# Kernel tuning notes

Hardware: AMD Instinct MI355X
Metric: run time of the kernel (lower is better)

The kernel has to match this reference:

```python
import jax, jax.numpy as jnp
import numpy as np

EPS = 1e-8


def corr1d(x, f, axis):
    """Centered 1-D correlation with filter f along `axis`, edge-padded."""
    k = f.shape[0]
    pad = k // 2
    padw = [(0, 0)] * x.ndim
    padw[axis] = (pad, pad)
    xp = jnp.pad(x, padw, mode='edge')
    n = x.shape[axis]
    out = jnp.zeros_like(x)
    for i in range(k):  # k is a small static filter size (3)
        sl = [slice(None)] * x.ndim
        sl[axis] = slice(i, i + n)
        out = out + f[i] * xp[tuple(sl)]
    return out


def conv2d_same(x, k2d):
    # x: [B,1,H,W], k2d: [kh,kw]
    return jax.lax.conv_general_dilated(x, k2d[None, None], (1, 1), 'SAME')


def setup_inputs() -> dict:
    key = jax.random.key(0)
    mosaick = jax.random.uniform(key, (16, 1, 1024, 1024), dtype=jnp.float32)
    # parameter inits exactly as in the torch module (sizes 3)
    gfilt = jnp.zeros((3,), jnp.float32).at[0].set(0.5).at[2].set(0.5)
    grad_filt = jnp.zeros((3,), jnp.float32).at[0].set(-1.0).at[2].set(1.0)
    return {"mosaick": mosaick, "gfilt": gfilt, "grad_filt": grad_filt}


def reference(mosaick, gfilt, grad_filt):
    m = mosaick  # [B,1,H,W], GRBG Bayer pattern
    B, _, H, W = m.shape
    yy, xx = jnp.meshgrid(jnp.arange(H), jnp.arange(W), indexing='ij')
    is_g = ((xx % 2) == (yy % 2)).astype(m.dtype)[None, None]          # green sites
    mask_r = (((yy % 2) == 0) & ((xx % 2) == 1)).astype(m.dtype)[None, None]
    mask_b = (((yy % 2) == 1) & ((xx % 2) == 0)).astype(m.dtype)[None, None]

    # learnable gradient measure (horizontal / vertical)
    dx = corr1d(m, grad_filt, axis=3)
    dy = corr1d(m, grad_filt, axis=2)
    # learnable green interpolation candidates
    gh = corr1d(m, gfilt, axis=3)
    gv = corr1d(m, gfilt, axis=2)

    adx, ady = jnp.abs(dx), jnp.abs(dy)
    w = ady / (adx + ady + EPS)          # big |dy| -> interpolate horizontally
    g_interp = w * gh + (1.0 - w) * gv
    green = is_g * m + (1.0 - is_g) * g_interp  # [B,1,H,W]

    # chroma reconstruction: bilinear interpolation of color differences
    K = jnp.array([[0.25, 0.5, 0.25],
                   [0.5, 1.0, 0.5],
                   [0.25, 0.5, 0.25]], m.dtype)

    def interp_chroma(mask):
        sparse = (m - green) * mask
        num = conv2d_same(sparse, K)
        den = conv2d_same(mask, K)  # mask is [1,1,H,W]; broadcasts in division
        return num / (den + EPS)

    red = green + interp_chroma(mask_r)
    blue = green + interp_chroma(mask_b)
    return jnp.concatenate([red, green, blue], axis=1)  # [B,3,H,W]
```

## Files before the change

kernel.cpp:

```cpp
#include <hip/hip_runtime.h>

#define HH 1024
#define WW 1024
#define TSX 128
#define TILE_H 64
#define ROWS_PW 16
#define SMW 134
#define SMH (TILE_H + 4)
#define EPSF 1e-8f

__device__ __forceinline__ float rcpf(float x) { return __builtin_amdgcn_rcpf(x); }

__global__ __launch_bounds__(256) void demosaick(
    const float* __restrict__ mos,
    const float* __restrict__ gfilt,
    const float* __restrict__ gradf,
    float* __restrict__ out)
{
    __shared__ __align__(16) float SM[SMH * SMW];
    const int tid  = threadIdx.x;
    const int lane = tid & 63;
    const int wv   = tid >> 6;
    const int bx = blockIdx.x, by = blockIdx.y, bz = blockIdx.z;
    const int gx0 = bx * TSX;
    const int gy0 = by * TILE_H;
    const size_t plane = (size_t)HH * WW;
    const float* __restrict__ src = mos + (size_t)bz * plane;

    const float gf0 = gfilt[0], gf1 = gfilt[1], gf2 = gfilt[2];
    const float df0 = gradf[0], df1 = gradf[1], df2 = gradf[2];

    for (int i = tid; i < SMH * (TSX + 4); i += 256) {
        int r = i / (TSX + 4);
        int c = i - r * (TSX + 4);
        int gy = min(max(gy0 - 2 + r, 0), HH - 1);
        int gx = min(max(gx0 - 2 + c, 0), WW - 1);
        SM[r * SMW + c] = src[(size_t)gy * WW + gx];
    }
    __syncthreads();

    const int ry0 = gy0 + wv * ROWS_PW;
    const int sr0 = wv * ROWS_PW;

    auto load_row = [&](int smr, float* d) {
        const float2* p = reinterpret_cast<const float2*>(&SM[smr * SMW + 2 * lane]);
        float2 a = p[0], b2 = p[1], c2 = p[2];
        d[0] = a.x; d[1] = a.y; d[2] = b2.x; d[3] = b2.y; d[4] = c2.x; d[5] = c2.y;
    };
    auto gi_at = [&](const float* up, const float* mid, const float* dn, int j) -> float {
        float xl = mid[j - 1], xc = mid[j], xr = mid[j + 1];
        float yu = up[j], yd = dn[j];
        float dx = df0 * xl + df1 * xc + df2 * xr;
        float dy = df0 * yu + df1 * xc + df2 * yd;
        float gh = gf0 * xl + gf1 * xc + gf2 * xr;
        float gv = gf0 * yu + gf1 * xc + gf2 * yd;
        float adx = fabsf(dx), ady = fabsf(dy);
        float w = ady * rcpf(adx + ady + EPSF);
        return w * gh + (1.0f - w) * gv;
    };
    auto green_row = [&](int gy, const float* up, const float* mid, const float* dn, float* G) {
        if (gy & 1) {
            G[0] = mid[1]; G[2] = mid[3];
            G[1] = gi_at(up, mid, dn, 2);
            G[3] = gi_at(up, mid, dn, 4);
        } else {
            G[1] = mid[2]; G[3] = mid[4];
            G[0] = gi_at(up, mid, dn, 1);
            G[2] = gi_at(up, mid, dn, 3);
        }
    };

    float A[6], Mm1[6], M0[6], Mp1[6], Mp2[6];
    float Gm1[4], G0[4], Gp1[4];
    load_row(sr0 + 0, A);
    load_row(sr0 + 1, Mm1);
    load_row(sr0 + 2, M0);
    load_row(sr0 + 3, Mp1);
    green_row(ry0 - 1, A, Mm1, M0, Gm1);
    green_row(ry0,     Mm1, M0, Mp1, G0);

    const int x0 = gx0 + 2 * lane;
    const float wL = (x0 - 1 >= 0) ? 1.0f : 0.0f;
    const float wR = (x0 + 2 < WW) ? 1.0f : 0.0f;
    float* __restrict__ obase = out + (size_t)bz * 3 * plane + (size_t)x0;

    #pragma unroll 4
    for (int r = 0; r < ROWS_PW; ++r) {
        const int y = ry0 + r;
        load_row(sr0 + r + 4, Mp2);
        green_row(y + 1, M0, Mp1, Mp2, Gp1);

        const float fU = (y > 0) ? 1.0f : 0.0f;
        const float fD = (y < HH - 1) ? 1.0f : 0.0f;
        const float g0 = G0[1], g1 = G0[2];
        const float m0 = M0[2], m1 = M0[3];
        float r0, b0, r1, b1;
        if ((y & 1) == 0) {
            {
                float dL = M0[1] - G0[0], dR = M0[3] - G0[2];
                r0 = g0 + (0.5f * (wL * dL + dR)) * rcpf(0.5f * (wL + 1.0f) + EPSF);
                float dU = Mm1[2] - Gm1[1], dD = Mp1[2] - Gp1[1];
                b0 = g0 + (0.5f * (fU * dU + fD * dD)) * rcpf(0.5f * (fU + fD) + EPSF);
            }
            {
                r1 = m1;
                float dUL = Mm1[2] - Gm1[1], dUR = Mm1[4] - Gm1[3];
                float dDL = Mp1[2] - Gp1[1], dDR = Mp1[4] - Gp1[3];
                float num = 0.25f * (fU * (dUL + wR * dUR) + fD * (dDL + wR * dDR));
                float den = 0.25f * ((fU + fD) * (1.0f + wR));
                b1 = g1 + num * rcpf(den + EPSF);
            }
        } else {
            {
                b0 = m0;
                float dUL = Mm1[1] - Gm1[0], dUR = Mm1[3] - Gm1[2];
                float dDL = Mp1[1] - Gp1[0], dDR = Mp1[3] - Gp1[2];
                float num = 0.25f * (fU * (wL * dUL + dUR) + fD * (wL * dDL + dDR));
                float den = 0.25f * ((fU + fD) * (wL + 1.0f));
                r0 = g0 + num * rcpf(den + EPSF);
            }
            {
                float dU = Mm1[3] - Gm1[2], dD = Mp1[3] - Gp1[2];
                r1 = g1 + (0.5f * (fU * dU + fD * dD)) * rcpf(0.5f * (fU + fD) + EPSF);
                float dL = M0[2] - G0[1], dR = M0[4] - G0[3];
                b1 = g1 + (0.5f * (dL + wR * dR)) * rcpf(0.5f * (1.0f + wR) + EPSF);
            }
        }

        float* prow = obase + (size_t)y * WW;
        *reinterpret_cast<float2*>(prow)             = make_float2(r0, r1);
        *reinterpret_cast<float2*>(prow + plane)     = make_float2(g0, g1);
        *reinterpret_cast<float2*>(prow + 2 * plane) = make_float2(b0, b1);

        #pragma unroll
        for (int j = 0; j < 6; ++j) { Mm1[j] = M0[j]; M0[j] = Mp1[j]; Mp1[j] = Mp2[j]; }
        #pragma unroll
        for (int j = 0; j < 4; ++j) { Gm1[j] = G0[j]; G0[j] = Gp1[j]; }
    }
}

extern "C" void kernel_launch(void* const* d_in, const int* in_sizes, int n_in,
                              void* d_out, int out_size, void* d_ws, size_t ws_size,
                              hipStream_t stream) {
    const float* mos = (const float*)d_in[0];
    const float* gf  = (const float*)d_in[1];
    const float* df  = (const float*)d_in[2];
    float* o = (float*)d_out;
    int B = in_sizes[0] / (HH * WW);
    dim3 grid(WW / TSX, HH / TILE_H, B);
    demosaick<<<grid, dim3(256, 1, 1), 0, stream>>>(mos, gf, df, o);
}
```

Before: 271.2 us.

## Drop shared-memory staging; read rows directly from global, 4 pixels per thread

Removes the LDS tile and its __syncthreads, so each thread loads its input rows straight from global memory as a float4 plus float2 halos, using a sliding register window over 16 rows. Each thread now produces 4 output pixels per row and writes them as float4 stores, and one block covers a full 1024-wide row strip. A launch-bounds occupancy hint is also added. The cost is redundant halo and row reads through cache (each row is read by overlapping strips), fewer and larger blocks, and more registers per thread.

```diff
diff --git a/kernel.cpp b/kernel.cpp
--- a/kernel.cpp
+++ b/kernel.cpp
@@ -2,51 +2,45 @@
 
 #define HH 1024
 #define WW 1024
-#define TSX 128
-#define TILE_H 64
-#define ROWS_PW 16
-#define SMW 134
-#define SMH (TILE_H + 4)
+#define ROWS 16
 #define EPSF 1e-8f
 
 __device__ __forceinline__ float rcpf(float x) { return __builtin_amdgcn_rcpf(x); }
 
-__global__ __launch_bounds__(256) void demosaick(
+__global__ __launch_bounds__(256, 4) void demosaick(
     const float* __restrict__ mos,
     const float* __restrict__ gfilt,
     const float* __restrict__ gradf,
     float* __restrict__ out)
 {
-    __shared__ __align__(16) float SM[SMH * SMW];
-    const int tid  = threadIdx.x;
-    const int lane = tid & 63;
-    const int wv   = tid >> 6;
-    const int bx = blockIdx.x, by = blockIdx.y, bz = blockIdx.z;
-    const int gx0 = bx * TSX;
-    const int gy0 = by * TILE_H;
+    const int tid = threadIdx.x;
+    const int x0  = tid * 4;
+    const int by = blockIdx.y, bz = blockIdx.z;
+    const int ry0 = by * ROWS;
     const size_t plane = (size_t)HH * WW;
     const float* __restrict__ src = mos + (size_t)bz * plane;
 
     const float gf0 = gfilt[0], gf1 = gfilt[1], gf2 = gfilt[2];
     const float df0 = gradf[0], df1 = gradf[1], df2 = gradf[2];
 
-    for (int i = tid; i < SMH * (TSX + 4); i += 256) {
-        int r = i / (TSX + 4);
-        int c = i - r * (TSX + 4);
-        int gy = min(max(gy0 - 2 + r, 0), HH - 1);
-        int gx = min(max(gx0 - 2 + c, 0), WW - 1);
-        SM[r * SMW + c] = src[(size_t)gy * WW + gx];
-    }
-    __syncthreads();
+    const bool eL = (x0 == 0);
+    const bool eR = (x0 == WW - 4);
+    const int bLc = eL ? 0 : x0 - 2;
+    const int bRc = eR ? WW - 2 : x0 + 4;
 
-    const int ry0 = gy0 + wv * ROWS_PW;
-    const int sr0 = wv * ROWS_PW;
+    auto load_mrow = [&](int y, float* w) {
+        int yy = min(max(y, 0), HH - 1);
+        const float* row = src + (size_t)yy * WW;
+        float4 q1 = *reinterpret_cast<const float4*>(row + x0);
+        float2 q0 = *reinterpret_cast<const float2*>(row + bLc);
+        float2 q2 = *reinterpret_cast<const float2*>(row + bRc);
+        w[2] = q1.x; w[3] = q1.y; w[4] = q1.z; w[5] = q1.w;
+        w[0] = eL ? q1.x : q0.x;
+        w[1] = eL ? q1.x : q0.y;
+        w[6] = eR ? q2.y : q2.x;
+        w[7] = q2.y;
+    };
 
-    auto load_row = [&](int smr, float* d) {
-        const float2* p = reinterpret_cast<const float2*>(&SM[smr * SMW + 2 * lane]);
-        float2 a = p[0], b2 = p[1], c2 = p[2];
-        d[0] = a.x; d[1] = a.y; d[2] = b2.x; d[3] = b2.y; d[4] = c2.x; d[5] = c2.y;
-    };
     auto gi_at = [&](const float* up, const float* mid, const float* dn, int j) -> float {
         float xl = mid[j - 1], xc = mid[j], xr = mid[j + 1];
         float yu = up[j], yd = dn[j];
@@ -58,84 +52,84 @@
         float w = ady * rcpf(adx + ady + EPSF);
         return w * gh + (1.0f - w) * gv;
     };
-    auto green_row = [&](int gy, const float* up, const float* mid, const float* dn, float* G) {
-        if (gy & 1) {
-            G[0] = mid[1]; G[2] = mid[3];
+    auto green_row = [&](int y, const float* up, const float* mid, const float* dn, float* G) {
+        if (y & 1) {
+            G[0] = mid[1]; G[2] = mid[3]; G[4] = mid[5];
             G[1] = gi_at(up, mid, dn, 2);
             G[3] = gi_at(up, mid, dn, 4);
+            G[5] = gi_at(up, mid, dn, 6);
         } else {
-            G[1] = mid[2]; G[3] = mid[4];
+            G[1] = mid[2]; G[3] = mid[4]; G[5] = mid[6];
             G[0] = gi_at(up, mid, dn, 1);
             G[2] = gi_at(up, mid, dn, 3);
+            G[4] = gi_at(up, mid, dn, 5);
         }
     };
 
-    float A[6], Mm1[6], M0[6], Mp1[6], Mp2[6];
-    float Gm1[4], G0[4], Gp1[4];
-    load_row(sr0 + 0, A);
-    load_row(sr0 + 1, Mm1);
-    load_row(sr0 + 2, M0);
-    load_row(sr0 + 3, Mp1);
-    green_row(ry0 - 1, A, Mm1, M0, Gm1);
+    float A8[8], Mm1[8], M0[8], Mp1[8], Mp2[8];
+    float Gm1[6], G0[6], Gp1[6];
+    load_mrow(ry0 - 2, A8);
+    load_mrow(ry0 - 1, Mm1);
+    load_mrow(ry0,     M0);
+    load_mrow(ry0 + 1, Mp1);
+    green_row(ry0 - 1, A8, Mm1, M0, Gm1);
     green_row(ry0,     Mm1, M0, Mp1, G0);
 
-    const int x0 = gx0 + 2 * lane;
-    const float wL = (x0 - 1 >= 0) ? 1.0f : 0.0f;
-    const float wR = (x0 + 2 < WW) ? 1.0f : 0.0f;
+    const float wl0 = eL ? 0.0f : 1.0f;
+    const float wr3 = eR ? 0.0f : 1.0f;
     float* __restrict__ obase = out + (size_t)bz * 3 * plane + (size_t)x0;
 
     #pragma unroll 4
-    for (int r = 0; r < ROWS_PW; ++r) {
+    for (int r = 0; r < ROWS; ++r) {
         const int y = ry0 + r;
-        load_row(sr0 + r + 4, Mp2);
+        load_mrow(y + 2, Mp2);
         green_row(y + 1, M0, Mp1, Mp2, Gp1);
 
         const float fU = (y > 0) ? 1.0f : 0.0f;
         const float fD = (y < HH - 1) ? 1.0f : 0.0f;
-        const float g0 = G0[1], g1 = G0[2];
-        const float m0 = M0[2], m1 = M0[3];
-        float r0, b0, r1, b1;
+
+        auto wl = [&](int p) -> float { return p == 0 ? wl0 : 1.0f; };
+        auto wr = [&](int p) -> float { return p == 3 ? wr3 : 1.0f; };
+        auto pair_h = [&](int p) -> float {
+            float dL = M0[p + 1] - G0[p], dR = M0[p + 3] - G0[p + 2];
+            float num = wl(p) * dL + wr(p) * dR;
+            float den = wl(p) + wr(p);
+            return G0[p + 1] + (0.5f * num) * rcpf(0.5f * den + EPSF);
+        };
+        auto pair_v = [&](int p) -> float {
+            float dU = Mm1[p + 2] - Gm1[p + 1], dD = Mp1[p + 2] - Gp1[p + 1];
+            return G0[p + 1] + (0.5f * (fU * dU + fD * dD)) * rcpf(0.5f * (fU + fD) + EPSF);
+        };
+        auto corners = [&](int p) -> float {
+            float dUL = Mm1[p + 1] - Gm1[p],     dUR = Mm1[p + 3] - Gm1[p + 2];
+            float dDL = Mp1[p + 1] - Gp1[p],     dDR = Mp1[p + 3] - Gp1[p + 2];
+            float num = 0.25f * (fU * (wl(p) * dUL + wr(p) * dUR) + fD * (wl(p) * dDL + wr(p) * dDR));
+            float den = 0.25f * ((fU + fD) * (wl(p) + wr(p)));
+            return G0[p + 1] + num * rcpf(den + EPSF);
+        };
+
+        float R[4], Bv[4];
         if ((y & 1) == 0) {
-            {
-                float dL = M0[1] - G0[0], dR = M0[3] - G0[2];
-                r0 = g0 + (0.5f * (wL * dL + dR)) * rcpf(0.5f * (wL + 1.0f) + EPSF);
-                float dU = Mm1[2] - Gm1[1], dD = Mp1[2] - Gp1[1];
-                b0 = g0 + (0.5f * (fU * dU + fD * dD)) * rcpf(0.5f * (fU + fD) + EPSF);
-            }
-            {
-                r1 = m1;
-                float dUL = Mm1[2] - Gm1[1], dUR = Mm1[4] - Gm1[3];
-                float dDL = Mp1[2] - Gp1[1], dDR = Mp1[4] - Gp1[3];
-                float num = 0.25f * (fU * (dUL + wR * dUR) + fD * (dDL + wR * dDR));
-                float den = 0.25f * ((fU + fD) * (1.0f + wR));
-                b1 = g1 + num * rcpf(den + EPSF);
-            }
+            R[0] = pair_h(0);  Bv[0] = pair_v(0);
+            R[1] = M0[3];      Bv[1] = corners(1);
+            R[2] = pair_h(2);  Bv[2] = pair_v(2);
+            R[3] = M0[5];      Bv[3] = corners(3);
         } else {
-            {
-                b0 = m0;
-                float dUL = Mm1[1] - Gm1[0], dUR = Mm1[3] - Gm1[2];
-                float dDL = Mp1[1] - Gp1[0], dDR = Mp1[3] - Gp1[2];
-                float num = 0.25f * (fU * (wL * dUL + dUR) + fD * (wL * dDL + dDR));
-                float den = 0.25f * ((fU + fD) * (wL + 1.0f));
-                r0 = g0 + num * rcpf(den + EPSF);
-            }
-            {
-                float dU = Mm1[3] - Gm1[2], dD = Mp1[3] - Gp1[2];
-                r1 = g1 + (0.5f * (fU * dU + fD * dD)) * rcpf(0.5f * (fU + fD) + EPSF);
-                float dL = M0[2] - G0[1], dR = M0[4] - G0[3];
-                b1 = g1 + (0.5f * (dL + wR * dR)) * rcpf(0.5f * (1.0f + wR) + EPSF);
-            }
+            R[0] = corners(0); Bv[0] = M0[2];
+            R[1] = pair_v(1);  Bv[1] = pair_h(1);
+            R[2] = corners(2); Bv[2] = M0[4];
+            R[3] = pair_v(3);  Bv[3] = pair_h(3);
         }
 
         float* prow = obase + (size_t)y * WW;
-        *reinterpret_cast<float2*>(prow)             = make_float2(r0, r1);
-        *reinterpret_cast<float2*>(prow + plane)     = make_float2(g0, g1);
-        *reinterpret_cast<float2*>(prow + 2 * plane) = make_float2(b0, b1);
+        *reinterpret_cast<float4*>(prow)             = make_float4(R[0], R[1], R[2], R[3]);
+        *reinterpret_cast<float4*>(prow + plane)     = make_float4(G0[1], G0[2], G0[3], G0[4]);
+        *reinterpret_cast<float4*>(prow + 2 * plane) = make_float4(Bv[0], Bv[1], Bv[2], Bv[3]);
 
         #pragma unroll
-        for (int j = 0; j < 6; ++j) { Mm1[j] = M0[j]; M0[j] = Mp1[j]; Mp1[j] = Mp2[j]; }
+        for (int j = 0; j < 8; ++j) { Mm1[j] = M0[j]; M0[j] = Mp1[j]; Mp1[j] = Mp2[j]; }
         #pragma unroll
-        for (int j = 0; j < 4; ++j) { Gm1[j] = G0[j]; G0[j] = Gp1[j]; }
+        for (int j = 0; j < 6; ++j) { Gm1[j] = G0[j]; G0[j] = Gp1[j]; }
     }
 }
 
@@ -147,6 +141,6 @@
     const float* df  = (const float*)d_in[2];
     float* o = (float*)d_out;
     int B = in_sizes[0] / (HH * WW);
-    dim3 grid(WW / TSX, HH / TILE_H, B);
+    dim3 grid(1, HH / ROWS, B);
     demosaick<<<grid, dim3(256, 1, 1), 0, stream>>>(mos, gf, df, o);
 }
```

Result: faster. 261.9 us (-3.4%).
